# Kernel tuning notes

Measured on AMD Instinct MI355X. Metric: run time of the kernel, lower is better.

The kernel has to match this reference:

```python
import jax, jax.numpy as jnp
import numpy as np

M, U, H, C, EMB, HID = 4096, 8, 8, 64, 64, 128
N = M * U            # 32768 nodes
E = 131072           # edges
D = H * C            # 512 = heads * hidden_channels
NUM_LAYERS = 4
IN0 = 6              # 2 coords + mask + speed + cost + arrival
SCALE = np.float32(1.0 / np.sqrt(C))

def _lin(x, W, b):
    return x @ W + b

def _transformer_conv(x, src, dst, Wq, bq, Wk, bk, Wv, bv, Ws, bs):
    # PyG TransformerConv: x_j = x[src], x_i = x[dst]; softmax over edges per dst
    n = x.shape[0]
    q = _lin(x, Wq, bq).reshape(n, H, C)
    k = _lin(x, Wk, bk).reshape(n, H, C)
    v = _lin(x, Wv, bv).reshape(n, H, C)
    alpha = jnp.einsum('ehc,ehc->eh', q[dst], k[src]) * SCALE   # [E,H]
    amax = jax.ops.segment_max(alpha, dst, num_segments=n)       # [N,H]
    ex = jnp.exp(alpha - amax[dst])
    denom = jax.ops.segment_sum(ex, dst, num_segments=n)         # [N,H]
    agg = jax.ops.segment_sum(ex[:, :, None] * v[src], dst, num_segments=n)  # [N,H,C]
    out = agg / (denom[:, :, None] + 1e-16)
    return out.reshape(n, D) + _lin(x, Ws, bs)                   # concat heads + root skip

def _forward(mission_coords, uavs_info, speeds, cost_matrix, arrival_times,
             Wq0, bq0, Wk0, bk0, Wv0, bv0, Ws0, bs0,
             Wq, bq, Wk, bk, Wv, bv, Ws, bs,
             fc_W, fc_b, aW1, ab1, aW2, ab2, cW1, cb1, cW2, cb2,
             edge_index, batch, action_mask):
    mc = jnp.broadcast_to(mission_coords[:, None, :], (M, U, 2))
    mk = jnp.broadcast_to(action_mask[:, None, None].astype(jnp.float32), (M, U, 1))
    sp = jnp.broadcast_to(speeds[None, :, None], (M, U, 1))
    cm = cost_matrix.T[:, :, None]
    at = arrival_times.T[:, :, None]
    x = jnp.concatenate([mc, mk, sp, cm, at], axis=-1).reshape(N, IN0)
    src, dst = edge_index[0], edge_index[1]
    x = jax.nn.relu(_transformer_conv(x, src, dst, Wq0, bq0, Wk0, bk0, Wv0, bv0, Ws0, bs0))
    for l in range(NUM_LAYERS - 1):
        x = jax.nn.relu(_transformer_conv(x, src, dst, Wq[l], bq[l], Wk[l], bk[l], Wv[l], bv[l], Ws[l], bs[l]))
    new_batch = jnp.repeat(batch, U)                             # [N]
    sums = jax.ops.segment_sum(x, new_batch, num_segments=1)
    cnts = jax.ops.segment_sum(jnp.ones((N,), x.dtype), new_batch, num_segments=1)
    pooled = sums / cnts[:, None]                                # [1, D]
    emb = _lin(pooled, fc_W, fc_b)                               # [1, EMB]
    emb_exp = jnp.tile(emb, (U, 1))                              # [U, EMB]
    combined = jnp.concatenate([uavs_info, emb_exp, speeds[:, None]], axis=-1)  # [U, EMB+3]
    action_probs = jax.nn.softmax(_lin(jax.nn.relu(_lin(combined, aW1, ab1)), aW2, ab2), axis=-1)
    state_values = _lin(jax.nn.relu(_lin(combined, cW1, cb1)), cW2, cb2)
    return action_probs, state_values

def setup_inputs() -> dict:
    key = jax.random.key(0)
    ks = jax.random.split(key, 40)
    def nrm(i, shape, s=0.05):
        return jax.random.normal(ks[i], shape, jnp.float32) * s
    z = lambda *s: jnp.zeros(s, jnp.float32)
    L = NUM_LAYERS - 1
    inp = dict(
        mission_coords=jax.random.uniform(ks[0], (M, 2), jnp.float32),
        uavs_info=nrm(1, (U, 2), 1.0),
        speeds=jax.random.uniform(ks[2], (U,), jnp.float32) + 0.5,
        cost_matrix=jax.random.uniform(ks[3], (U, M), jnp.float32),
        arrival_times=jax.random.uniform(ks[4], (U, M), jnp.float32),
        edge_index=jax.random.randint(ks[5], (2, E), 0, N),
        batch=jnp.zeros((M,), jnp.int32),
        action_mask=jax.random.randint(ks[6], (M,), 0, 2),
        Wq0=nrm(7, (IN0, D)), bq0=z(D), Wk0=nrm(8, (IN0, D)), bk0=z(D),
        Wv0=nrm(9, (IN0, D)), bv0=z(D), Ws0=nrm(10, (IN0, D)), bs0=z(D),
        Wq=nrm(11, (L, D, D)), bq=z(L, D), Wk=nrm(12, (L, D, D)), bk=z(L, D),
        Wv=nrm(13, (L, D, D)), bv=z(L, D), Ws=nrm(14, (L, D, D)), bs=z(L, D),
        fc_W=nrm(15, (D, EMB)), fc_b=z(EMB),
        aW1=nrm(16, (EMB + 3, HID)), ab1=z(HID), aW2=nrm(17, (HID, M)), ab2=z(M),
        cW1=nrm(18, (EMB + 3, HID)), cb1=z(HID), cW2=nrm(19, (HID, 1)), cb2=z(1),
    )
    return inp

def reference(mission_coords, edge_index, batch, uavs_info, action_mask, speeds,
              cost_matrix, arrival_times,
              Wq0, bq0, Wk0, bk0, Wv0, bv0, Ws0, bs0,
              Wq, bq, Wk, bk, Wv, bv, Ws, bs,
              fc_W, fc_b, aW1, ab1, aW2, ab2, cW1, cb1, cW2, cb2):
    return _forward(mission_coords, uavs_info, speeds, cost_matrix, arrival_times,
                    Wq0, bq0, Wk0, bk0, Wv0, bv0, Ws0, bs0,
                    Wq, bq, Wk, bk, Wv, bv, Ws, bs,
                    fc_W, fc_b, aW1, ab1, aW2, ab2, cW1, cb1, cW2, cb2,
                    edge_index, batch, action_mask)
```

## Files before the change

### kernel.cpp

```cpp
#include <hip/hip_runtime.h>
#include <stdint.h>

typedef unsigned char u8;
typedef unsigned short u16;
typedef unsigned long long u64;
typedef __attribute__((ext_vector_type(8))) unsigned short u16x8;
typedef __attribute__((ext_vector_type(8))) __bf16 bf16x8;
typedef __attribute__((ext_vector_type(4))) float f32x4;
typedef __attribute__((ext_vector_type(2))) float f32x2;

#define NNODES 32768
#define NEDGES 131072
#define DDIM 512
#define QK4 2048
#define MM 4096
#define UU 8


__device__ __forceinline__ u16 f2bf(float f) {
    unsigned u = __builtin_bit_cast(unsigned, f);
    u += 0x7FFFu + ((u >> 16) & 1u);
    return (u16)(u >> 16);
}
__device__ __forceinline__ float bf2f(u16 h) {
    return __builtin_bit_cast(float, (unsigned)h << 16);
}
__device__ __forceinline__ void enc8(const float* f, int* lo, int* hi) {
    int a = __builtin_amdgcn_cvt_pk_fp8_f32(f[0], f[1], 0, false);
    a = __builtin_amdgcn_cvt_pk_fp8_f32(f[2], f[3], a, true);
    int b = __builtin_amdgcn_cvt_pk_fp8_f32(f[4], f[5], 0, false);
    b = __builtin_amdgcn_cvt_pk_fp8_f32(f[6], f[7], b, true);
    *lo = a;
    *hi = b;
}
__device__ __forceinline__ void dec8(int lo, int hi, float* f) {
    f32x2 a = __builtin_amdgcn_cvt_pk_f32_fp8(lo, false);
    f32x2 b = __builtin_amdgcn_cvt_pk_f32_fp8(lo, true);
    f32x2 c = __builtin_amdgcn_cvt_pk_f32_fp8(hi, false);
    f32x2 d = __builtin_amdgcn_cvt_pk_f32_fp8(hi, true);
    f[0] = a[0]; f[1] = a[1]; f[2] = b[0]; f[3] = b[1];
    f[4] = c[0]; f[5] = c[1]; f[6] = d[0]; f[7] = d[1];
}

__device__ __forceinline__ void load_lds16(const void* g, void* l) {
    __builtin_amdgcn_global_load_lds((__attribute__((address_space(1))) unsigned int*)(void*)g,
                                     (__attribute__((address_space(3))) unsigned int*)l, 16, 0, 0);
}

__global__ void k_prep(const float* __restrict__ mc, const int* __restrict__ mask,
                       const float* __restrict__ sp, const float* __restrict__ cm,
                       const float* __restrict__ at, float* __restrict__ x0,
                       const float* __restrict__ bq, const float* __restrict__ bk,
                       const float* __restrict__ bv, const float* __restrict__ bs,
                       float* __restrict__ bcat,
                       int* __restrict__ deg, float* __restrict__ pooled) {
    int b = blockIdx.x;
    int t = threadIdx.x;
    if (b < 128) {
        int node = b * 256 + t;
        deg[node] = 0;
        int m = node >> 3, u = node & 7;
        float* o = x0 + (size_t)node * 6;
        o[0] = mc[m * 2];
        o[1] = mc[m * 2 + 1];
        o[2] = (float)mask[m];
        o[3] = sp[u];
        o[4] = cm[u * MM + m];
        o[5] = at[u * MM + m];
    } else if (b < 152) {
        int i = (b - 128) * 256 + t;
        int n = i & (QK4 - 1);
        int l = i >> 11;
        const float* p;
        int col;
        if (n < 512) { p = bq; col = n; }
        else if (n < 1536) {
            int g = n - 512, c = g >> 4, r = g & 15;
            if (r < 8) { p = bk; col = c * 8 + r; }
            else { p = bv; col = c * 8 + r - 8; }
        } else { p = bs; col = n - 1536; }
        bcat[(size_t)l * QK4 + n] = p[l * DDIM + col];
    } else {
        pooled[(b - 152) * 256 + t] = 0.f;
    }
}

__global__ void k_c0(const float* __restrict__ Wq0, const float* __restrict__ bq0,
                     const float* __restrict__ Wk0, const float* __restrict__ bk0,
                     float* __restrict__ C0) {
    int i = threadIdx.x;
    if (i >= 392) return;
    int h = i / 49, r = i % 49;
    int d0 = h * 64;
    float s = 0.f;
    if (r < 36) {
        int a = r / 6, b = r % 6;
        for (int d = 0; d < 64; d++) s += Wq0[a * DDIM + d0 + d] * Wk0[b * DDIM + d0 + d];
    } else if (r < 42) {
        int a = r - 36;
        for (int d = 0; d < 64; d++) s += Wq0[a * DDIM + d0 + d] * bk0[d0 + d];
    } else if (r < 48) {
        int b = r - 42;
        for (int d = 0; d < 64; d++) s += Wk0[b * DDIM + d0 + d] * bq0[d0 + d];
    } else {
        for (int d = 0; d < 64; d++) s += bq0[d0 + d] * bk0[d0 + d];
    }
    C0[i] = s;
}

__global__ void k_wt(const float* __restrict__ Wq, const float* __restrict__ Wk,
                     const float* __restrict__ Wv, const float* __restrict__ Ws,
                     u16* __restrict__ Wt) {
    __shared__ float tile[32][33];
    int q = blockIdx.z;
    int l = q >> 2, t = q & 3;
    const float* src = ((t == 0) ? Wq : (t == 1) ? Wk : (t == 2) ? Wv : Ws) + (size_t)l * DDIM * DDIM;
    int k0 = blockIdx.x * 32, n0 = blockIdx.y * 32;
    int tx = threadIdx.x, ty = threadIdx.y;
#pragma unroll
    for (int r = 0; r < 4; r++) tile[ty + 8 * r][tx] = src[(size_t)(k0 + ty + 8 * r) * DDIM + n0 + tx];
    __syncthreads();
    u16* dst = Wt + (size_t)l * QK4 * DDIM;
#pragma unroll
    for (int r = 0; r < 4; r++) {
        int nn = n0 + ty + 8 * r;
        int n;
        if (t == 0) n = nn;
        else if (t == 1) n = 512 + ((nn >> 3) << 4) + (nn & 7);
        else if (t == 2) n = 512 + ((nn >> 3) << 4) + 8 + (nn & 7);
        else n = 1536 + nn;
        dst[(size_t)n * DDIM + k0 + tx] = f2bf(tile[tx][ty + 8 * r]);
    }
}

__global__ void k_count(const int* __restrict__ dst, int* __restrict__ deg) {
    int e = blockIdx.x * 256 + threadIdx.x;
    if (e < NEDGES) atomicAdd(&deg[dst[e]], 1);
}

__global__ __launch_bounds__(1024) void k_scan(const int* __restrict__ deg, int* __restrict__ offs,
                                               int* __restrict__ cursor) {
    __shared__ int sums[1024];
    int t = threadIdx.x;
    int base = t * 32;
    int local[32];
    int s = 0;
#pragma unroll
    for (int i = 0; i < 32; i++) { local[i] = s; s += deg[base + i]; }
    sums[t] = s;
    __syncthreads();
    for (int d = 1; d < 1024; d <<= 1) {
        int v = (t >= d) ? sums[t - d] : 0;
        __syncthreads();
        sums[t] += v;
        __syncthreads();
    }
    int excl = (t == 0) ? 0 : sums[t - 1];
#pragma unroll
    for (int i = 0; i < 32; i++) {
        int o = excl + local[i];
        offs[base + i] = o;
        cursor[base + i] = o;
    }
    if (t == 1023) offs[NNODES] = sums[1023];
}

__global__ void k_scatter(const int* __restrict__ src, const int* __restrict__ dst,
                          int* __restrict__ cursor, int* __restrict__ ssrc) {
    int e = blockIdx.x * 256 + threadIdx.x;
    if (e < NEDGES) {
        int pos = atomicAdd(&cursor[dst[e]], 1);
        ssrc[pos] = src[e];
    }
}

__global__ __launch_bounds__(256) void k_attn0(const float* __restrict__ x0, const float* __restrict__ C0,
                                               const float* __restrict__ Wv0, const float* __restrict__ bv0,
                                               const float* __restrict__ Ws0, const float* __restrict__ bs0,
                                               const int* __restrict__ offs, const int* __restrict__ ssrc,
                                               u16* __restrict__ Xout) {
    const int lane = threadIdx.x & 63;
    const int wv = threadIdx.x >> 6;
    const int h = lane & 7;
    float wV[8][6], wS[8][6], bV[8], bS[8];
#pragma unroll
    for (int j = 0; j < 8; ++j) {
        int c = lane + 64 * j;
        bV[j] = bv0[c];
        bS[j] = bs0[c];
#pragma unroll
        for (int a = 0; a < 6; ++a) {
            wV[j][a] = Wv0[a * DDIM + c];
            wS[j][a] = Ws0[a * DDIM + c];
        }
    }
    float Ah[36], uh[6], wh[6], ch;
#pragma unroll
    for (int r = 0; r < 36; ++r) Ah[r] = C0[h * 49 + r];
#pragma unroll
    for (int a = 0; a < 6; ++a) uh[a] = C0[h * 49 + 36 + a];
#pragma unroll
    for (int a = 0; a < 6; ++a) wh[a] = C0[h * 49 + 42 + a];
    ch = C0[h * 49 + 48];

    int node0 = (blockIdx.x * 4 + wv) * 8;
    for (int nn = 0; nn < 8; ++nn) {
        int node = node0 + nn;
        float xi[6];
#pragma unroll
        for (int a = 0; a < 6; ++a) xi[a] = x0[(size_t)node * 6 + a];
        float m = -INFINITY, l = 0.f;
        float xh[6];
#pragma unroll
        for (int a = 0; a < 6; ++a) xh[a] = 0.f;
        const int e0 = offs[node], e1 = offs[node + 1];
        for (int e = e0; e < e1; ++e) {
            int s = ssrc[e];
            float xj[6];
#pragma unroll
            for (int a = 0; a < 6; ++a) xj[a] = x0[(size_t)s * 6 + a];
            float alpha = ch;
#pragma unroll
            for (int a = 0; a < 6; ++a) {
                float t = uh[a];
#pragma unroll
                for (int b = 0; b < 6; ++b) t += Ah[a * 6 + b] * xj[b];
                alpha += xi[a] * t;
            }
#pragma unroll
            for (int b = 0; b < 6; ++b) alpha += wh[b] * xj[b];
            alpha *= 0.125f;
            float nm = fmaxf(m, alpha);
            float corr = __expf(m - nm);
            float p = __expf(alpha - nm);
            l = l * corr + p;
#pragma unroll
            for (int a = 0; a < 6; ++a) xh[a] = xh[a] * corr + p * xj[a];
            m = nm;
        }
#pragma unroll
        for (int j = 0; j < 8; ++j) {
            float lb = __shfl(l, j, 64);
            float num = lb * bV[j];
#pragma unroll
            for (int a = 0; a < 6; ++a) num += __shfl(xh[a], j, 64) * wV[j][a];
            float skip = bS[j];
#pragma unroll
            for (int a = 0; a < 6; ++a) skip += xi[a] * wS[j][a];
            float r = num / (lb + 1e-16f) + skip;
            Xout[(size_t)node * DDIM + lane + 64 * j] = f2bf(fmaxf(r, 0.f));
        }
    }
}

__global__ __launch_bounds__(256, 4) void k_gemm(const u16* __restrict__ X, const u16* __restrict__ Wt,
                                                 const float* __restrict__ bcat, u8* __restrict__ Q8,
                                                 u8* __restrict__ KV8, u16* __restrict__ S16) {
    __shared__ __align__(16) u16 smem[2 * 128 * 64];
    u16* As = smem;
    u16* Bs = smem + 128 * 64;
    const int tid = threadIdx.x;
    const int lane = tid & 63;
    const int w = tid >> 6;
    const int wm = w & 1, wn = w >> 1;
    const int bid = blockIdx.x;
    const int xcd = bid & 7;
    const int s = bid >> 3;
    const size_t arow0 = (size_t)(xcd * 32 + (s >> 4)) * 128;
    const size_t brow0 = (size_t)(s & 15) * 128;
    const int bt = (int)(brow0 >> 7);

    f32x4 acc[4][4];
#pragma unroll
    for (int i = 0; i < 4; i++)
#pragma unroll
        for (int j = 0; j < 4; j++) acc[i][j] = (f32x4){0.f, 0.f, 0.f, 0.f};

    const int la = lane & 7;
    const int quad = lane >> 4;
    const int lm = lane & 15;

    for (int kt = 0; kt < 8; ++kt) {
        const int k0 = kt * 64;
#pragma unroll
        for (int t = 0; t < 4; ++t) {
            int idx = (w * 4 + t) * 64 + lane;
            int m = idx >> 3;
            int c = la ^ (m & 7);
            const u16* ga = X + (arow0 + m) * DDIM + (k0 + c * 8);
            const u16* gb = Wt + (brow0 + m) * DDIM + (k0 + c * 8);
            load_lds16(ga, &As[(size_t)((w * 4 + t) * 64) * 8]);
            load_lds16(gb, &Bs[(size_t)((w * 4 + t) * 64) * 8]);
        }
        __syncthreads();
#pragma unroll
        for (int kk = 0; kk < 2; ++kk) {
            bf16x8 af[4], bfg[4];
            int c = kk * 4 + quad;
#pragma unroll
            for (int i = 0; i < 4; ++i) {
                int m = wm * 64 + i * 16 + lm;
                int slot = m * 8 + (c ^ (m & 7));
                af[i] = *(const bf16x8*)&As[(size_t)slot * 8];
            }
#pragma unroll
            for (int j = 0; j < 4; ++j) {
                int n = wn * 64 + j * 16 + lm;
                int slot = n * 8 + (c ^ (n & 7));
                bfg[j] = *(const bf16x8*)&Bs[(size_t)slot * 8];
            }
#pragma unroll
            for (int i = 0; i < 4; ++i)
#pragma unroll
                for (int j = 0; j < 4; ++j)
                    acc[i][j] = __builtin_amdgcn_mfma_f32_16x16x32_bf16(af[i], bfg[j], acc[i][j], 0, 0, 0);
        }
        __syncthreads();
    }

    float biasv[4];
#pragma unroll
    for (int j = 0; j < 4; ++j) biasv[j] = bcat[brow0 + wn * 64 + j * 16 + lm];

    u16* stg = smem;
    const int chunk = lane & 7;
    const int rrow = lane >> 3;
    const int colbase = (int)brow0 + wn * 64 + chunk * 8;
#pragma unroll
    for (int p = 0; p < 2; ++p) {
        __syncthreads();
#pragma unroll
        for (int ii = 0; ii < 2; ++ii) {
            int i = p * 2 + ii;
#pragma unroll
            for (int j = 0; j < 4; ++j) {
#pragma unroll
                for (int r = 0; r < 4; ++r) {
                    int lr = ii * 16 + quad * 4 + r;
                    int lc = j * 16 + lm;
                    stg[(size_t)(w * 32 + lr) * 72 + lc] = f2bf(acc[i][j][r] + biasv[j]);
                }
            }
        }
        __syncthreads();
#pragma unroll
        for (int it = 0; it < 4; ++it) {
            int row = it * 8 + rrow;
            u16x8 v = *(const u16x8*)&stg[(size_t)(w * 32 + row) * 72 + chunk * 8];
            size_t grow = arow0 + wm * 64 + p * 32 + row;
            if (bt < 4) {
                float f[8];
#pragma unroll
                for (int j = 0; j < 8; j++) f[j] = bf2f(v[j]);
                int lo, hi;
                enc8(f, &lo, &hi);
                *(int2*)(Q8 + grow * 512 + colbase) = make_int2(lo, hi);
            } else if (bt < 12) {
                float f[8];
#pragma unroll
                for (int j = 0; j < 8; j++) f[j] = bf2f(v[j]);
                int lo, hi;
                enc8(f, &lo, &hi);
                *(int2*)(KV8 + grow * 1024 + (colbase - 512)) = make_int2(lo, hi);
            } else {
                *(u16x8*)(S16 + grow * 512 + (colbase - 1536)) = v;
            }
        }
    }
}

__global__ __launch_bounds__(256) void k_attn(const u8* __restrict__ Q8, const u8* __restrict__ KV8,
                                              const u16* __restrict__ S16, const int* __restrict__ offs,
                                              const int* __restrict__ ssrc, u16* __restrict__ Xout) {
    const int lane = threadIdx.x & 63;
    const int node = blockIdx.x * 4 + (threadIdx.x >> 6);
    const u64 q8 = *(const u64*)(Q8 + (size_t)node * 512 + (size_t)lane * 8);
    const u16x8 sv = *(const u16x8*)(S16 + (size_t)node * 512 + (size_t)lane * 8);
    float qf[8];
    dec8((int)(q8 & 0xFFFFFFFFull), (int)(q8 >> 32), qf);
    float m = -INFINITY, l = 0.f;
    float acc[8];
#pragma unroll
    for (int j = 0; j < 8; j++) acc[j] = 0.f;
    const int e0 = offs[node], e1 = offs[node + 1];
    int e = e0;
    while (e < e1) {
        int nb = e1 - e;
        if (nb > 4) nb = 4;
        int4 kvb[4];
#pragma unroll
        for (int i = 0; i < 4; ++i) {
            if (i < nb) {
                int s = ssrc[e + i];
                kvb[i] = *(const int4*)(KV8 + (size_t)s * 1024 + (size_t)lane * 16);
            }
        }
#pragma unroll
        for (int i = 0; i < 4; ++i) {
            if (i >= nb) break;
            int4 kv = kvb[i];
            f32x2 k01 = __builtin_amdgcn_cvt_pk_f32_fp8(kv.x, false);
            f32x2 k23 = __builtin_amdgcn_cvt_pk_f32_fp8(kv.x, true);
            f32x2 k45 = __builtin_amdgcn_cvt_pk_f32_fp8(kv.y, false);
            f32x2 k67 = __builtin_amdgcn_cvt_pk_f32_fp8(kv.y, true);
            float d = qf[0] * k01[0] + qf[1] * k01[1] + qf[2] * k23[0] + qf[3] * k23[1] +
                      qf[4] * k45[0] + qf[5] * k45[1] + qf[6] * k67[0] + qf[7] * k67[1];
            d += __shfl_xor(d, 1, 64);
            d += __shfl_xor(d, 2, 64);
            d += __shfl_xor(d, 4, 64);
            float a = d * 0.125f;
            float nm = fmaxf(m, a);
            float corr = __expf(m - nm);
            float p = __expf(a - nm);
            l = l * corr + p;
            f32x2 v01 = __builtin_amdgcn_cvt_pk_f32_fp8(kv.z, false);
            f32x2 v23 = __builtin_amdgcn_cvt_pk_f32_fp8(kv.z, true);
            f32x2 v45 = __builtin_amdgcn_cvt_pk_f32_fp8(kv.w, false);
            f32x2 v67 = __builtin_amdgcn_cvt_pk_f32_fp8(kv.w, true);
            acc[0] = acc[0] * corr + p * v01[0];
            acc[1] = acc[1] * corr + p * v01[1];
            acc[2] = acc[2] * corr + p * v23[0];
            acc[3] = acc[3] * corr + p * v23[1];
            acc[4] = acc[4] * corr + p * v45[0];
            acc[5] = acc[5] * corr + p * v45[1];
            acc[6] = acc[6] * corr + p * v67[0];
            acc[7] = acc[7] * corr + p * v67[1];
            m = nm;
        }
        e += nb;
    }
    float inv = 1.0f / (l + 1e-16f);
    u16x8 o;
#pragma unroll
    for (int j = 0; j < 8; j++) {
        float r = acc[j] * inv + bf2f(sv[j]);
        o[j] = f2bf(fmaxf(r, 0.f));
    }
    *(u16x8*)(Xout + (size_t)node * DDIM + (size_t)lane * 8) = o;
}

__global__ __launch_bounds__(256) void k_pool(const u16* __restrict__ X, float* __restrict__ pooled) {
    __shared__ float red[4][64][8];
    int t = threadIdx.x;
    int chunk = t & 63;
    int rofs = t >> 6;
    float s[8];
#pragma unroll
    for (int j = 0; j < 8; j++) s[j] = 0.f;
    int nd0 = blockIdx.x * 256;
    for (int nd = nd0 + rofs; nd < nd0 + 256; nd += 4) {
        u16x8 v = *(const u16x8*)&X[(size_t)nd * DDIM + chunk * 8];
#pragma unroll
        for (int j = 0; j < 8; j++) s[j] += bf2f(v[j]);
    }
#pragma unroll
    for (int j = 0; j < 8; j++) red[rofs][chunk][j] = s[j];
    __syncthreads();
    if (t < 64) {
#pragma unroll
        for (int j = 0; j < 8; j++) {
            float o = red[0][t][j] + red[1][t][j] + red[2][t][j] + red[3][t][j];
            atomicAdd(&pooled[t * 8 + j], o);
        }
    }
}

__global__ __launch_bounds__(1024) void k_heads(const float* __restrict__ pooled, const float* __restrict__ fcW,
                                                const float* __restrict__ fcb, const float* __restrict__ ui,
                                                const float* __restrict__ sp, const float* __restrict__ aW1,
                                                const float* __restrict__ ab1, const float* __restrict__ cW1,
                                                const float* __restrict__ cb1, const float* __restrict__ cW2,
                                                const float* __restrict__ cb2, float* __restrict__ hidden_a,
                                                float* __restrict__ out) {
    __shared__ float spool[512];
    __shared__ float semb[64];
    __shared__ float shc[8][128];
    int t = threadIdx.x;
    if (t < 512) spool[t] = pooled[t] * (1.0f / 32768.0f);
    __syncthreads();
    if (t < 64) {
        float s = fcb[t];
        for (int k = 0; k < 512; k++) s += spool[k] * fcW[k * 64 + t];
        semb[t] = s;
    }
    __syncthreads();
    int u = t >> 7, j = t & 127;
    float u0 = ui[u * 2], u1 = ui[u * 2 + 1], uspd = sp[u];
    float ha = ab1[j] + u0 * aW1[j] + u1 * aW1[128 + j] + uspd * aW1[66 * 128 + j];
    float hc = cb1[j] + u0 * cW1[j] + u1 * cW1[128 + j] + uspd * cW1[66 * 128 + j];
    for (int k = 0; k < 64; k++) {
        float e = semb[k];
        ha += e * aW1[(2 + k) * 128 + j];
        hc += e * cW1[(2 + k) * 128 + j];
    }
    ha = fmaxf(ha, 0.f);
    hc = fmaxf(hc, 0.f);
    hidden_a[u * 128 + j] = ha;
    shc[u][j] = hc;
    __syncthreads();
    if (t < 8) {
        float s = cb2[0];
        for (int k = 0; k < 128; k++) s += shc[t][k] * cW2[k];
        out[NNODES + t] = s;
    }
}

__global__ __launch_bounds__(1024) void k_actor(const float* __restrict__ hidden_a, const float* __restrict__ aW2,
                                                const float* __restrict__ ab2, float* __restrict__ out) {
    __shared__ float h[128];
    __shared__ float red[1024];
    int u = blockIdx.x, t = threadIdx.x;
    if (t < 128) h[t] = hidden_a[u * 128 + t];
    __syncthreads();
    float lg[4];
#pragma unroll
    for (int p = 0; p < 4; p++) {
        int mcol = t + p * 1024;
        float s = ab2[mcol];
        for (int k = 0; k < 128; k++) s += h[k] * aW2[(size_t)k * MM + mcol];
        lg[p] = s;
    }
    float mx = fmaxf(fmaxf(lg[0], lg[1]), fmaxf(lg[2], lg[3]));
    red[t] = mx;
    __syncthreads();
    for (int s2 = 512; s2 > 0; s2 >>= 1) {
        if (t < s2) red[t] = fmaxf(red[t], red[t + s2]);
        __syncthreads();
    }
    mx = red[0];
    __syncthreads();
    float e[4], sum = 0.f;
#pragma unroll
    for (int p = 0; p < 4; p++) {
        e[p] = __expf(lg[p] - mx);
        sum += e[p];
    }
    red[t] = sum;
    __syncthreads();
    for (int s2 = 512; s2 > 0; s2 >>= 1) {
        if (t < s2) red[t] += red[t + s2];
        __syncthreads();
    }
    float inv = 1.0f / red[0];
#pragma unroll
    for (int p = 0; p < 4; p++) out[(size_t)u * MM + t + p * 1024] = e[p] * inv;
}

extern "C" void kernel_launch(void* const* d_in, const int* in_sizes, int n_in,
                              void* d_out, int out_size, void* d_ws, size_t ws_size,
                              hipStream_t stream) {
    const float* mc   = (const float*)d_in[0];
    const float* ui   = (const float*)d_in[1];
    const float* sp   = (const float*)d_in[2];
    const float* cm   = (const float*)d_in[3];
    const float* at   = (const float*)d_in[4];
    const int*   eidx = (const int*)d_in[5];
    const int*   mask = (const int*)d_in[7];
    const float* Wq0 = (const float*)d_in[8];
    const float* bq0 = (const float*)d_in[9];
    const float* Wk0 = (const float*)d_in[10];
    const float* bk0 = (const float*)d_in[11];
    const float* Wv0 = (const float*)d_in[12];
    const float* bv0 = (const float*)d_in[13];
    const float* Ws0 = (const float*)d_in[14];
    const float* bs0 = (const float*)d_in[15];
    const float* Wq = (const float*)d_in[16];
    const float* bq = (const float*)d_in[17];
    const float* Wk = (const float*)d_in[18];
    const float* bk = (const float*)d_in[19];
    const float* Wv = (const float*)d_in[20];
    const float* bv = (const float*)d_in[21];
    const float* Ws = (const float*)d_in[22];
    const float* bs = (const float*)d_in[23];
    const float* fcW = (const float*)d_in[24];
    const float* fcb = (const float*)d_in[25];
    const float* aW1 = (const float*)d_in[26];
    const float* ab1 = (const float*)d_in[27];
    const float* aW2 = (const float*)d_in[28];
    const float* ab2 = (const float*)d_in[29];
    const float* cW1 = (const float*)d_in[30];
    const float* cb1 = (const float*)d_in[31];
    const float* cW2 = (const float*)d_in[32];
    const float* cb2 = (const float*)d_in[33];
    float* out = (float*)d_out;

    const int* esrc = eidx;
    const int* edst = eidx + NEDGES;

    char* ws = (char*)d_ws;
    size_t off = 0;
    auto alloc = [&](size_t bytes) -> void* {
        void* p = ws + off;
        off += (bytes + 255) & ~(size_t)255;
        return p;
    };
    u8*    Q8    = (u8*)alloc((size_t)NNODES * 512);
    u8*    KV8   = (u8*)alloc((size_t)NNODES * 1024);
    u16*   S16   = (u16*)alloc((size_t)NNODES * 512 * 2);
    u16*   X     = (u16*)alloc((size_t)NNODES * DDIM * 2);
    u16*   Wt    = (u16*)alloc((size_t)3 * QK4 * DDIM * 2);
    float* bcat  = (float*)alloc((size_t)3 * QK4 * 4);
    float* C0    = (float*)alloc((size_t)392 * 4);
    float* x0    = (float*)alloc((size_t)NNODES * 6 * 4);
    int*   deg   = (int*)alloc((size_t)NNODES * 4);
    int*   offs  = (int*)alloc((size_t)(NNODES + 1) * 4);
    int*   cursor= (int*)alloc((size_t)NNODES * 4);
    int*   ssrc  = (int*)alloc((size_t)NEDGES * 4);
    float* pooled= (float*)alloc((size_t)512 * 4);
    float* hidden_a = (float*)alloc((size_t)UU * 128 * 4);
    (void)ws_size; (void)in_sizes; (void)n_in; (void)out_size;

    k_prep<<<154, 256, 0, stream>>>(mc, mask, sp, cm, at, x0, bq, bk, bv, bs, bcat, deg, pooled);
    k_c0<<<1, 512, 0, stream>>>(Wq0, bq0, Wk0, bk0, C0);
    {
        dim3 g(16, 16, 12), b(32, 8);
        k_wt<<<g, b, 0, stream>>>(Wq, Wk, Wv, Ws, Wt);
    }
    k_count<<<NEDGES / 256, 256, 0, stream>>>(edst, deg);
    k_scan<<<1, 1024, 0, stream>>>(deg, offs, cursor);
    k_scatter<<<NEDGES / 256, 256, 0, stream>>>(esrc, edst, cursor, ssrc);

    k_attn0<<<1024, 256, 0, stream>>>(x0, C0, Wv0, bv0, Ws0, bs0, offs, ssrc, X);

    for (int l = 0; l < 3; ++l) {
        k_gemm<<<4096, 256, 0, stream>>>(X, Wt + (size_t)l * QK4 * DDIM, bcat + (size_t)l * QK4, Q8, KV8, S16);
        k_attn<<<NNODES / 4, 256, 0, stream>>>(Q8, KV8, S16, offs, ssrc, X);
    }

    k_pool<<<128, 256, 0, stream>>>(X, pooled);
    k_heads<<<1, 1024, 0, stream>>>(pooled, fcW, fcb, ui, sp, aW1, ab1, cW1, cb1, cW2, cb2, hidden_a, out);
    k_actor<<<UU, 1024, 0, stream>>>(hidden_a, aW2, ab2, out);
}
```

Baseline: 618.5 us.

## Process eight nodes per wave in parallel in layer-0 attention with prefetch

The layer-0 attention kernel previously walked its 8 nodes one after another, with only 8 of 64 lanes (one per head) doing the edge softmax. It now assigns each 8-lane group to a different node, so all 64 lanes run the online softmax at once, looping up to the wave's maximum degree with masking. The next neighbor's features are prefetched one edge ahead. Results are redistributed by shuffles for the output projection, which adds masked iterations whenever node degrees differ within a wave.

New measurement: 594.0 us (median of 2 runs). 1.04x faster.

```diff
diff --git a/kernel.cpp b/kernel.cpp
--- a/kernel.cpp
+++ b/kernel.cpp
@@ -181,6 +181,7 @@
                                                u16* __restrict__ Xout) {
     const int lane = threadIdx.x & 63;
     const int wv = threadIdx.x >> 6;
+    const int g = lane >> 3;
     const int h = lane & 7;
     float wV[8][6], wS[8][6], bV[8], bS[8];
 #pragma unroll
@@ -203,52 +204,73 @@
     for (int a = 0; a < 6; ++a) wh[a] = C0[h * 49 + 42 + a];
     ch = C0[h * 49 + 48];
 
-    int node0 = (blockIdx.x * 4 + wv) * 8;
+    const int node0 = (blockIdx.x * 4 + wv) * 8;
+    const int node = node0 + g;
+    float xi[6];
+#pragma unroll
+    for (int a = 0; a < 6; ++a) xi[a] = x0[(size_t)node * 6 + a];
+    const int e0 = offs[node];
+    const int deg = offs[node + 1] - e0;
+    int dmax = deg;
+    dmax = max(dmax, __shfl_xor(dmax, 8, 64));
+    dmax = max(dmax, __shfl_xor(dmax, 16, 64));
+    dmax = max(dmax, __shfl_xor(dmax, 32, 64));
+
+    float m = -1e30f, l = 0.f;
+    float xh[6];
+#pragma unroll
+    for (int a = 0; a < 6; ++a) xh[a] = 0.f;
+    float xj[6];
+    {
+        int s = (deg > 0) ? ssrc[e0] : 0;
+#pragma unroll
+        for (int a = 0; a < 6; ++a) xj[a] = x0[(size_t)s * 6 + a];
+    }
+    for (int e = 0; e < dmax; ++e) {
+        float xc[6];
+#pragma unroll
+        for (int a = 0; a < 6; ++a) xc[a] = xj[a];
+        const bool act = (e < deg);
+        int sn = (e + 1 < deg) ? ssrc[e0 + e + 1] : 0;
+#pragma unroll
+        for (int a = 0; a < 6; ++a) xj[a] = x0[(size_t)sn * 6 + a];
+        float alpha = ch;
+#pragma unroll
+        for (int a = 0; a < 6; ++a) {
+            float t = uh[a];
+#pragma unroll
+            for (int b = 0; b < 6; ++b) t += Ah[a * 6 + b] * xc[b];
+            alpha += xi[a] * t;
+        }
+#pragma unroll
+        for (int b = 0; b < 6; ++b) alpha += wh[b] * xc[b];
+        alpha *= 0.125f;
+        float nm = act ? fmaxf(m, alpha) : m;
+        float corr = __expf(m - nm);
+        float p = act ? __expf(alpha - nm) : 0.f;
+        l = l * corr + p;
+#pragma unroll
+        for (int a = 0; a < 6; ++a) xh[a] = xh[a] * corr + p * xc[a];
+        m = nm;
+    }
+#pragma unroll
     for (int nn = 0; nn < 8; ++nn) {
-        int node = node0 + nn;
-        float xi[6];
-#pragma unroll
-        for (int a = 0; a < 6; ++a) xi[a] = x0[(size_t)node * 6 + a];
-        float m = -INFINITY, l = 0.f;
-        float xh[6];
-#pragma unroll
-        for (int a = 0; a < 6; ++a) xh[a] = 0.f;
-        const int e0 = offs[node], e1 = offs[node + 1];
-        for (int e = e0; e < e1; ++e) {
-            int s = ssrc[e];
-            float xj[6];
-#pragma unroll
-            for (int a = 0; a < 6; ++a) xj[a] = x0[(size_t)s * 6 + a];
-            float alpha = ch;
-#pragma unroll
-            for (int a = 0; a < 6; ++a) {
-                float t = uh[a];
-#pragma unroll
-                for (int b = 0; b < 6; ++b) t += Ah[a * 6 + b] * xj[b];
-                alpha += xi[a] * t;
-            }
-#pragma unroll
-            for (int b = 0; b < 6; ++b) alpha += wh[b] * xj[b];
-            alpha *= 0.125f;
-            float nm = fmaxf(m, alpha);
-            float corr = __expf(m - nm);
-            float p = __expf(alpha - nm);
-            l = l * corr + p;
-#pragma unroll
-            for (int a = 0; a < 6; ++a) xh[a] = xh[a] * corr + p * xj[a];
-            m = nm;
-        }
+        int dnode = node0 + nn;
+        float xin[6];
+#pragma unroll
+        for (int a = 0; a < 6; ++a) xin[a] = __shfl(xi[a], nn * 8, 64);
 #pragma unroll
         for (int j = 0; j < 8; ++j) {
-            float lb = __shfl(l, j, 64);
+            int srcl = nn * 8 + j;
+            float lb = __shfl(l, srcl, 64);
             float num = lb * bV[j];
 #pragma unroll
-            for (int a = 0; a < 6; ++a) num += __shfl(xh[a], j, 64) * wV[j][a];
+            for (int a = 0; a < 6; ++a) num += __shfl(xh[a], srcl, 64) * wV[j][a];
             float skip = bS[j];
 #pragma unroll
-            for (int a = 0; a < 6; ++a) skip += xi[a] * wS[j][a];
+            for (int a = 0; a < 6; ++a) skip += xin[a] * wS[j][a];
             float r = num / (lb + 1e-16f) + skip;
-            Xout[(size_t)node * DDIM + lane + 64 * j] = f2bf(fmaxf(r, 0.f));
+            Xout[(size_t)dnode * DDIM + lane + 64 * j] = f2bf(fmaxf(r, 0.f));
         }
     }
 }
```
